# Kernel tuning notes

Hardware: AMD Instinct MI355X
Metric: run time of the kernel (lower is better)

The kernel has to match this reference:

```python
import jax, jax.numpy as jnp
from jax import lax
import numpy as np

B, N, C = 8, 32768, 256          # batch, num votes, seed_feat_dim
P, S = 256, 16                   # num_proposal, nsample
RADIUS = 0.3
NH, NS, NC = 1, 18, 18           # heading bins, size clusters, classes
OUT_DIM = 2 + 3 + NH * 2 + NS * 4 + NC  # 97
BN_EPS = 1e-3                    # keras BatchNormalization default epsilon
BN_SCALE = np.float32(1.0 / np.sqrt(1.0 + BN_EPS))  # moving_mean=0, moving_var=1
MEAN_SIZE = ((np.arange(NS * 3, dtype=np.float32).reshape(NS, 3) % 5.0) + 1.0) * 0.2


def _bn(x, g, b):
    # inference-mode BN with moving_mean=0, moving_var=1
    return g * (x * BN_SCALE) + b


def _fps(xyz, npoint):
    # farthest point sampling -> [B, npoint] int32 indices
    b, n = xyz.shape[0], xyz.shape[1]

    def step(carry, _):
        dist, last = carry                                   # [B,N], [B]
        p = jnp.take_along_axis(xyz, last[:, None, None], axis=1)  # [B,1,3]
        d = jnp.sum((xyz - p) ** 2, axis=-1)                 # [B,N]
        dist = jnp.minimum(dist, d)
        nxt = jnp.argmax(dist, axis=1).astype(jnp.int32)
        return (dist, nxt), last

    init = (jnp.full((b, n), 1e10, xyz.dtype), jnp.zeros((b,), jnp.int32))
    _, inds = lax.scan(step, init, None, length=npoint)
    return jnp.transpose(inds)                               # [B, npoint]


def _ball_query(xyz, new_xyz, radius, nsample):
    # first-nsample neighbors within radius, padded with first hit -> [B,P,S]
    n = xyz.shape[1]
    d2 = (jnp.sum(new_xyz ** 2, -1)[:, :, None]
          + jnp.sum(xyz ** 2, -1)[:, None, :]
          - 2.0 * jnp.einsum('bpd,bnd->bpn', new_xyz, xyz))  # [B,P,N]
    key = jnp.where(d2 < radius * radius, jnp.arange(n, dtype=jnp.int32), n)
    sel = -lax.top_k(-key, nsample)[0]                        # ascending smallest
    first = sel[..., :1]                                      # query point itself is always in-radius
    return jnp.where(sel < n, sel, first)


def _forward(xyz, features, mw0, mb0, mg0, me0, mw1, mb1, mg1, me1,
             mw2, mb2, mg2, me2, hw1, hb1, hg1, he1, hw2, hb2, hg2, he2, hw3, hb3):
    fps_inds = _fps(xyz, P)                                           # [B,P]
    new_xyz = jnp.take_along_axis(xyz, fps_inds[..., None], axis=1)   # [B,P,3]
    idx = _ball_query(xyz, new_xyz, RADIUS, S)                        # [B,P,S]

    g_xyz = jax.vmap(lambda pts, i: pts[i])(xyz, idx)                 # [B,P,S,3]
    g_xyz = (g_xyz - new_xyz[:, :, None, :]) / RADIUS                 # normalize_xyz
    g_feat = jax.vmap(lambda f, i: f[i])(features, idx)               # [B,P,S,C]
    h = jnp.concatenate([g_xyz, g_feat], axis=-1)                     # [B,P,S,C+3]

    # shared MLP (conv2d 1x1 + BN + ReLU) then max-pool over samples
    h = jax.nn.relu(_bn(h @ mw0 + mb0, mg0, me0))
    h = jax.nn.relu(_bn(h @ mw1 + mb1, mg1, me1))
    h = jax.nn.relu(_bn(h @ mw2 + mb2, mg2, me2))
    feats = jnp.max(h, axis=2)                                        # [B,P,128]

    # proposal head: conv1x1 + BN + ReLU x2, then conv1x1
    net = jax.nn.relu(_bn(feats @ hw1 + hb1, hg1, he1))
    net = jax.nn.relu(_bn(net @ hw2 + hb2, hg2, he2))
    net = net @ hw3 + hb3                                             # [B,P,97]

    # decode_scores
    obj = net[:, :, 0:2]
    center = new_xyz + net[:, :, 2:5]
    hs = net[:, :, 5:5 + NH]
    hrn = net[:, :, 5 + NH:5 + 2 * NH]
    hr = hrn * (np.pi / NH)
    ss = net[:, :, 5 + 2 * NH:5 + 2 * NH + NS]
    srn = net[:, :, 5 + 2 * NH + NS:5 + 2 * NH + 4 * NS].reshape(net.shape[0], P, NS, 3)
    sr = srn * jnp.asarray(MEAN_SIZE)[None, None]
    sem = net[:, :, 5 + 2 * NH + 4 * NS:]
    return (obj, center, hs, hrn, hr, ss, srn, sr, sem)


def setup_inputs() -> dict:
    key = jax.random.key(0)
    ks = jax.random.split(key, 16)

    def w(k, shape, scale=0.05):
        return jax.random.normal(k, shape, jnp.float32) * scale

    z, o = jnp.zeros, jnp.ones
    return {
        'xyz': jax.random.normal(ks[0], (B, N, 3), jnp.float32),
        'features': jax.random.normal(ks[1], (B, N, C), jnp.float32),
        'mw0': w(ks[2], (C + 3, 128)), 'mb0': z((128,)), 'mg0': o((128,)), 'me0': z((128,)),
        'mw1': w(ks[3], (128, 128)), 'mb1': z((128,)), 'mg1': o((128,)), 'me1': z((128,)),
        'mw2': w(ks[4], (128, 128)), 'mb2': z((128,)), 'mg2': o((128,)), 'me2': z((128,)),
        'hw1': w(ks[5], (128, 128)), 'hb1': z((128,)), 'hg1': o((128,)), 'he1': z((128,)),
        'hw2': w(ks[6], (128, 128)), 'hb2': z((128,)), 'hg2': o((128,)), 'he2': z((128,)),
        'hw3': w(ks[7], (128, OUT_DIM)), 'hb3': z((OUT_DIM,)),
    }


def reference(xyz, features, mw0, mb0, mg0, me0, mw1, mb1, mg1, me1,
              mw2, mb2, mg2, me2, hw1, hb1, hg1, he1, hw2, hb2, hg2, he2, hw3, hb3):
    return _forward(xyz, features, mw0, mb0, mg0, me0, mw1, mb1, mg1, me1,
                    mw2, mb2, mg2, me2, hw1, hb1, hg1, he1, hw2, hb2, hg2, he2, hw3, hb3)
```

## Files before the change

kernel.cpp:

```cpp
#include <hip/hip_runtime.h>
#include <math.h>

#define NBATCH 8
#define NPOINT 32768
#define NFEAT 256
#define NPROP 256
#define NSAMP 16
#define KIN 259
#define HDIM 128
#define ODIM 97

__device__ __forceinline__ float addrn(float a, float b) {
  float r; asm("v_add_f32 %0, %1, %2" : "=v"(r) : "v"(a), "v"(b)); return r;
}
__device__ __forceinline__ float subrn(float a, float b) {
  float r; asm("v_sub_f32 %0, %1, %2" : "=v"(r) : "v"(a), "v"(b)); return r;
}

__global__ __launch_bounds__(512)
void fps_kernel(const float* __restrict__ xyz, int* __restrict__ fpsi,
                float* __restrict__ cxyz) {
  __shared__ __align__(16) float dist[NPOINT];
  __shared__ float rv[8];
  __shared__ int ri[8];
  __shared__ int bc;
  const int b = blockIdx.x;
  const int t = threadIdx.x;
  const float* __restrict__ Xp = xyz + (size_t)b * NPOINT * 3;
  float px[64], py[64], pz[64];
#pragma unroll
  for (int q = 0; q < 16; ++q) {
#pragma unroll
    for (int u = 0; u < 4; ++u) {
      const int i = q * 2048 + t * 4 + u;
      px[q*4+u] = Xp[3*i+0];
      py[q*4+u] = Xp[3*i+1];
      pz[q*4+u] = Xp[3*i+2];
    }
    *(float4*)&dist[q*2048 + t*4] = make_float4(1e10f, 1e10f, 1e10f, 1e10f);
  }
  __syncthreads();
  int last = 0;
  for (int step = 0; step < NPROP; ++step) {
    const float qx = Xp[3*last+0];
    const float qy = Xp[3*last+1];
    const float qz = Xp[3*last+2];
    if (t == 0) {
      fpsi[b*NPROP + step] = last;
      cxyz[(b*NPROP+step)*3+0] = qx;
      cxyz[(b*NPROP+step)*3+1] = qy;
      cxyz[(b*NPROP+step)*3+2] = qz;
    }
    float bv = -1.0f; int bi = 0;
#pragma unroll
    for (int q = 0; q < 16; ++q) {
      float4 dv = *(float4*)&dist[q*2048 + t*4];
      float* dp = (float*)&dv;
#pragma unroll
      for (int u = 0; u < 4; ++u) {
        const int j = q*4+u;
        const float dx = px[j]-qx, dy = py[j]-qy, dz = pz[j]-qz;
        const float d = addrn(addrn(dx*dx, dy*dy), dz*dz);
        const float nd = fminf(dp[u], d);
        dp[u] = nd;
        if (nd > bv) { bv = nd; bi = q*2048 + t*4 + u; }
      }
      *(float4*)&dist[q*2048 + t*4] = dv;
    }
#pragma unroll
    for (int m = 1; m < 64; m <<= 1) {
      const float ov = __shfl_xor(bv, m);
      const int   oi = __shfl_xor(bi, m);
      if (ov > bv || (ov == bv && oi < bi)) { bv = ov; bi = oi; }
    }
    if ((t & 63) == 0) { rv[t >> 6] = bv; ri[t >> 6] = bi; }
    __syncthreads();
    if (t < 64) {
      float fv = (t < 8) ? rv[t] : -2.0f;
      int   fi = (t < 8) ? ri[t] : 0x7fffffff;
#pragma unroll
      for (int m = 1; m < 8; m <<= 1) {
        const float ov = __shfl_xor(fv, m);
        const int   oi = __shfl_xor(fi, m);
        if (ov > fv || (ov == fv && oi < fi)) { fv = ov; fi = oi; }
      }
      if (t == 0) bc = fi;
    }
    __syncthreads();
    last = bc;
  }
}

__global__ __launch_bounds__(512)
void ballq_kernel(const float* __restrict__ xyz, const float* __restrict__ cxyz,
                  int* __restrict__ idx) {
  const int gw = (blockIdx.x * 512 + threadIdx.x) >> 6;
  const int lane = threadIdx.x & 63;
  const int b = gw >> 8;
  const float* __restrict__ Xp = xyz + (size_t)b * NPOINT * 3;
  const float cx = cxyz[gw*3+0], cy = cxyz[gw*3+1], cz = cxyz[gw*3+2];
  const float a = addrn(addrn(cx*cx, cy*cy), cz*cz);
  const float R2 = (float)(0.3 * 0.3);
  int* __restrict__ out = idx + gw * NSAMP;
  int cnt = 0, first = -1;
  for (int base = 0; base < NPOINT; base += 64) {
    const int i = base + lane;
    const float x = Xp[3*i+0], y = Xp[3*i+1], z = Xp[3*i+2];
    const float bb2 = addrn(addrn(x*x, y*y), z*z);
    const float cc  = addrn(addrn(cx*x, cy*y), cz*z);
    const float d2  = subrn(addrn(a, bb2), 2.0f*cc);
    const bool isin = d2 < R2;
    const unsigned long long m = __ballot(isin);
    if (m) {
      if (first < 0) first = base + (int)__builtin_ctzll(m);
      if (isin) {
        const int pos = cnt + (int)__builtin_popcountll(m & ((1ull << lane) - 1ull));
        if (pos < NSAMP) out[pos] = i;
      }
      cnt += (int)__builtin_popcountll(m);
      if (cnt >= NSAMP) break;
    }
  }
  if (lane < NSAMP && lane >= cnt) out[lane] = first;
}

__global__ __launch_bounds__(256)
void mlp0_kernel(const float* __restrict__ xyz, const float* __restrict__ feat,
                 const float* __restrict__ cxyz, const int* __restrict__ idx,
                 const float* __restrict__ W, const float* __restrict__ bias_,
                 const float* __restrict__ gam_, const float* __restrict__ bet_,
                 float* __restrict__ h0) {
  __shared__ __align__(16) float w[KIN*132];
  __shared__ __align__(16) float xs[16*264];
  __shared__ int ids[16];
  const int t = threadIdx.x;
  for (int i = t; i < KIN*HDIM; i += 256) {
    const int k = i >> 7, c = i & 127;
    w[k*132 + c] = W[i];
  }
  const int r  = t >> 4;
  const int c8 = (t & 15) * 8;
  float bs[8], gm[8], bt[8];
#pragma unroll
  for (int j = 0; j < 8; ++j) { bs[j] = bias_[c8+j]; gm[j] = gam_[c8+j]; bt[j] = bet_[c8+j]; }
  const float bns = (float)(1.0 / sqrt(1.001));
  for (int gi = 0; gi < 8; ++gi) {
    const int g = blockIdx.x * 8 + gi;
    const int b = g >> 8;
    __syncthreads();
    if (t < 16) ids[t] = idx[g*16 + t];
    __syncthreads();
#pragma unroll
    for (int s = 0; s < 16; ++s)
      xs[s*264 + 3 + t] = feat[((size_t)b*NPOINT + ids[s])*NFEAT + t];
    if (t < 48) {
      const int s = t / 3, d = t - 3*(t/3);
      const float v = xyz[((size_t)b*NPOINT + ids[s])*3 + d];
      xs[s*264 + d] = (v - cxyz[g*3 + d]) / 0.3f;
    }
    __syncthreads();
    float acc[8];
#pragma unroll
    for (int j = 0; j < 8; ++j) acc[j] = bs[j];
    for (int k = 0; k < KIN; ++k) {
      const float xv = xs[r*264 + k];
      const float4 wa = *(const float4*)&w[k*132 + c8];
      const float4 wb = *(const float4*)&w[k*132 + c8 + 4];
      acc[0] += xv*wa.x; acc[1] += xv*wa.y; acc[2] += xv*wa.z; acc[3] += xv*wa.w;
      acc[4] += xv*wb.x; acc[5] += xv*wb.y; acc[6] += xv*wb.z; acc[7] += xv*wb.w;
    }
    float ov[8];
#pragma unroll
    for (int j = 0; j < 8; ++j) ov[j] = fmaxf(gm[j]*(acc[j]*bns)+bt[j], 0.0f);
    float* dst = &h0[((size_t)g*16 + r)*HDIM + c8];
    *(float4*)&dst[0] = make_float4(ov[0],ov[1],ov[2],ov[3]);
    *(float4*)&dst[4] = make_float4(ov[4],ov[5],ov[6],ov[7]);
  }
}

__global__ __launch_bounds__(256)
void mlp12_kernel(const float* __restrict__ h0,
                  const float* __restrict__ W1, const float* __restrict__ b1,
                  const float* __restrict__ g1, const float* __restrict__ e1,
                  const float* __restrict__ W2, const float* __restrict__ b2,
                  const float* __restrict__ g2, const float* __restrict__ e2,
                  float* __restrict__ feats) {
  __shared__ __align__(16) float w1[HDIM*132];
  __shared__ __align__(16) float w2[HDIM*132];
  __shared__ __align__(16) float xs[16*132];
  __shared__ __align__(16) float ys[16*132];
  const int t = threadIdx.x;
  for (int i = t; i < HDIM*HDIM; i += 256) {
    const int k = i >> 7, c = i & 127;
    w1[k*132+c] = W1[i];
    w2[k*132+c] = W2[i];
  }
  const int r  = t >> 4;
  const int c8 = (t & 15) * 8;
  float bs1[8], gm1[8], bt1[8], bs2[8], gm2[8], bt2[8];
#pragma unroll
  for (int j = 0; j < 8; ++j) {
    bs1[j]=b1[c8+j]; gm1[j]=g1[c8+j]; bt1[j]=e1[c8+j];
    bs2[j]=b2[c8+j]; gm2[j]=g2[c8+j]; bt2[j]=e2[c8+j];
  }
  const float bns = (float)(1.0 / sqrt(1.001));
  for (int gi = 0; gi < 8; ++gi) {
    const int g = blockIdx.x * 8 + gi;
    __syncthreads();
    for (int i = t; i < 16*HDIM; i += 256) {
      const int s = i >> 7, k = i & 127;
      xs[s*132+k] = h0[((size_t)g*16 + s)*HDIM + k];
    }
    __syncthreads();
    float acc[8];
#pragma unroll
    for (int j = 0; j < 8; ++j) acc[j] = bs1[j];
#pragma unroll 4
    for (int k = 0; k < HDIM; ++k) {
      const float xv = xs[r*132 + k];
      const float4 wa = *(const float4*)&w1[k*132 + c8];
      const float4 wb = *(const float4*)&w1[k*132 + c8 + 4];
      acc[0]+=xv*wa.x; acc[1]+=xv*wa.y; acc[2]+=xv*wa.z; acc[3]+=xv*wa.w;
      acc[4]+=xv*wb.x; acc[5]+=xv*wb.y; acc[6]+=xv*wb.z; acc[7]+=xv*wb.w;
    }
    {
      float ov[8];
#pragma unroll
      for (int j = 0; j < 8; ++j) ov[j] = fmaxf(gm1[j]*(acc[j]*bns)+bt1[j], 0.0f);
      *(float4*)&ys[r*132 + c8]     = make_float4(ov[0],ov[1],ov[2],ov[3]);
      *(float4*)&ys[r*132 + c8 + 4] = make_float4(ov[4],ov[5],ov[6],ov[7]);
    }
    __syncthreads();
#pragma unroll
    for (int j = 0; j < 8; ++j) acc[j] = bs2[j];
#pragma unroll 4
    for (int k = 0; k < HDIM; ++k) {
      const float xv = ys[r*132 + k];
      const float4 wa = *(const float4*)&w2[k*132 + c8];
      const float4 wb = *(const float4*)&w2[k*132 + c8 + 4];
      acc[0]+=xv*wa.x; acc[1]+=xv*wa.y; acc[2]+=xv*wa.z; acc[3]+=xv*wa.w;
      acc[4]+=xv*wb.x; acc[5]+=xv*wb.y; acc[6]+=xv*wb.z; acc[7]+=xv*wb.w;
    }
    {
      float ov[8];
#pragma unroll
      for (int j = 0; j < 8; ++j) ov[j] = fmaxf(gm2[j]*(acc[j]*bns)+bt2[j], 0.0f);
      *(float4*)&xs[r*132 + c8]     = make_float4(ov[0],ov[1],ov[2],ov[3]);
      *(float4*)&xs[r*132 + c8 + 4] = make_float4(ov[4],ov[5],ov[6],ov[7]);
    }
    __syncthreads();
#pragma unroll
    for (int hh = 8; hh >= 1; hh >>= 1) {
      if (r < hh) {
#pragma unroll
        for (int j = 0; j < 8; ++j)
          xs[r*132 + c8 + j] = fmaxf(xs[r*132 + c8 + j], xs[(r+hh)*132 + c8 + j]);
      }
      __syncthreads();
    }
    if (r == 0) {
      *(float4*)&feats[(size_t)g*HDIM + c8]     = *(float4*)&xs[c8];
      *(float4*)&feats[(size_t)g*HDIM + c8 + 4] = *(float4*)&xs[c8+4];
    }
  }
}

__global__ __launch_bounds__(256)
void head_kernel(const float* __restrict__ in_, const float* __restrict__ W,
                 const float* __restrict__ b_, const float* __restrict__ g_,
                 const float* __restrict__ e_, float* __restrict__ out_) {
  __shared__ __align__(16) float w[HDIM*132];
  __shared__ __align__(16) float xs[16*132];
  const int t = threadIdx.x;
  for (int i = t; i < HDIM*HDIM; i += 256) {
    const int k = i >> 7, c = i & 127;
    w[k*132+c] = W[i];
  }
  const int row0 = blockIdx.x * 16;
  for (int i = t; i < 16*HDIM; i += 256) {
    const int s = i >> 7, k = i & 127;
    xs[s*132+k] = in_[((size_t)row0 + s)*HDIM + k];
  }
  const int r  = t >> 4;
  const int c8 = (t & 15) * 8;
  float bs[8], gm[8], bt[8];
#pragma unroll
  for (int j = 0; j < 8; ++j) { bs[j]=b_[c8+j]; gm[j]=g_[c8+j]; bt[j]=e_[c8+j]; }
  const float bns = (float)(1.0 / sqrt(1.001));
  __syncthreads();
  float acc[8];
#pragma unroll
  for (int j = 0; j < 8; ++j) acc[j] = bs[j];
#pragma unroll 4
  for (int k = 0; k < HDIM; ++k) {
    const float xv = xs[r*132 + k];
    const float4 wa = *(const float4*)&w[k*132 + c8];
    const float4 wb = *(const float4*)&w[k*132 + c8 + 4];
    acc[0]+=xv*wa.x; acc[1]+=xv*wa.y; acc[2]+=xv*wa.z; acc[3]+=xv*wa.w;
    acc[4]+=xv*wb.x; acc[5]+=xv*wb.y; acc[6]+=xv*wb.z; acc[7]+=xv*wb.w;
  }
  float ov[8];
#pragma unroll
  for (int j = 0; j < 8; ++j) ov[j] = fmaxf(gm[j]*(acc[j]*bns)+bt[j], 0.0f);
  float* dst = &out_[((size_t)row0 + r)*HDIM + c8];
  *(float4*)&dst[0] = make_float4(ov[0],ov[1],ov[2],ov[3]);
  *(float4*)&dst[4] = make_float4(ov[4],ov[5],ov[6],ov[7]);
}

__global__ __launch_bounds__(128)
void head3_kernel(const float* __restrict__ net2, const float* __restrict__ W3,
                  const float* __restrict__ b3, const float* __restrict__ cxyz,
                  float* __restrict__ out) {
  __shared__ float x[HDIM];
  const int g = blockIdx.x;
  const int t = threadIdx.x;
  x[t] = net2[(size_t)g*HDIM + t];
  __syncthreads();
  if (t >= ODIM) return;
  float acc = b3[t];
#pragma unroll 4
  for (int k = 0; k < HDIM; ++k) acc += x[k] * W3[k*ODIM + t];
  const int OBJ=0, CEN=4096, HSo=10240, HRN=12288, HRo=14336,
            SSo=16384, SRN=53248, SRo=163840, SEM=274432;
  if (t < 2)       out[OBJ + g*2 + t] = acc;
  else if (t < 5)  out[CEN + g*3 + (t-2)] = acc + cxyz[g*3 + (t-2)];
  else if (t == 5) out[HSo + g] = acc;
  else if (t == 6) { out[HRN + g] = acc; out[HRo + g] = acc * (float)M_PI; }
  else if (t < 25) out[SSo + g*18 + (t-7)] = acc;
  else if (t < 79) {
    const int m2 = t - 25;
    out[SRN + g*54 + m2] = acc;
    out[SRo + g*54 + m2] = acc * ((float)(m2 % 5 + 1) * 0.2f);
  }
  else             out[SEM + g*18 + (t-79)] = acc;
}

extern "C" void kernel_launch(void* const* d_in, const int* in_sizes, int n_in,
                              void* d_out, int out_size, void* d_ws, size_t ws_size,
                              hipStream_t stream) {
  (void)in_sizes; (void)n_in; (void)out_size; (void)ws_size;
  const float* xyz  = (const float*)d_in[0];
  const float* feat = (const float*)d_in[1];
  const float* mw0 = (const float*)d_in[2];
  const float* mb0 = (const float*)d_in[3];
  const float* mg0 = (const float*)d_in[4];
  const float* me0 = (const float*)d_in[5];
  const float* mw1 = (const float*)d_in[6];
  const float* mb1 = (const float*)d_in[7];
  const float* mg1 = (const float*)d_in[8];
  const float* me1 = (const float*)d_in[9];
  const float* mw2 = (const float*)d_in[10];
  const float* mb2 = (const float*)d_in[11];
  const float* mg2 = (const float*)d_in[12];
  const float* me2 = (const float*)d_in[13];
  const float* hw1 = (const float*)d_in[14];
  const float* hb1 = (const float*)d_in[15];
  const float* hg1 = (const float*)d_in[16];
  const float* he1 = (const float*)d_in[17];
  const float* hw2 = (const float*)d_in[18];
  const float* hb2 = (const float*)d_in[19];
  const float* hg2 = (const float*)d_in[20];
  const float* he2 = (const float*)d_in[21];
  const float* hw3 = (const float*)d_in[22];
  const float* hb3 = (const float*)d_in[23];
  float* out = (float*)d_out;
  char* ws = (char*)d_ws;
  int*   fpsi = (int*)(ws + 0);
  float* cxyz = (float*)(ws + 8192);
  int*   idx  = (int*)(ws + 32768);
  float* h0   = (float*)(ws + 163840);
  float* fts  = (float*)(ws + 16941056);
  float* net1 = (float*)(ws + 17989632);
  float* net2 = (float*)(ws + 19038208);

  fps_kernel<<<NBATCH, 512, 0, stream>>>(xyz, fpsi, cxyz);
  ballq_kernel<<<256, 512, 0, stream>>>(xyz, cxyz, idx);
  mlp0_kernel<<<256, 256, 0, stream>>>(xyz, feat, cxyz, idx, mw0, mb0, mg0, me0, h0);
  mlp12_kernel<<<256, 256, 0, stream>>>(h0, mw1, mb1, mg1, me1, mw2, mb2, mg2, me2, fts);
  head_kernel<<<128, 256, 0, stream>>>(fts, hw1, hb1, hg1, he1, net1);
  head_kernel<<<128, 256, 0, stream>>>(net1, hw2, hb2, hg2, he2, net2);
  head3_kernel<<<2048, 128, 0, stream>>>(net2, hw3, hb3, cxyz, out);
}
```

Before: 1.284 ms.

## Convert xyz to SoA buffers and widen FPS blocks to 1024 threads

Adds a pre-pass that splits the interleaved xyz array into separate x, y and z arrays in workspace. FPS and ball query then read them with coalesced, vectorized float4 loads and single-element lookups instead of strided loads. FPS now uses 1024 threads per batch, so each thread holds 32 points instead of 64 and the cross-wave reduction covers 16 waves. The cost is an extra kernel launch plus the SoA write and read traffic. The SoA buffers alias the h0 region, which is written only later by mlp0, and the unused fps index output is dropped.

```diff
diff --git a/kernel.cpp b/kernel.cpp
--- a/kernel.cpp
+++ b/kernel.cpp
@@ -17,44 +17,55 @@
   float r; asm("v_sub_f32 %0, %1, %2" : "=v"(r) : "v"(a), "v"(b)); return r;
 }
 
-__global__ __launch_bounds__(512)
-void fps_kernel(const float* __restrict__ xyz, int* __restrict__ fpsi,
-                float* __restrict__ cxyz) {
+__global__ __launch_bounds__(256)
+void soa_kernel(const float* __restrict__ xyz, float* __restrict__ xs,
+                float* __restrict__ ys, float* __restrict__ zs) {
+  const int i = blockIdx.x * 256 + threadIdx.x;
+  xs[i] = xyz[3*i+0];
+  ys[i] = xyz[3*i+1];
+  zs[i] = xyz[3*i+2];
+}
+
+__global__ __launch_bounds__(1024, 4)
+void fps_kernel(const float* __restrict__ xs_, const float* __restrict__ ys_,
+                const float* __restrict__ zs_, float* __restrict__ cxyz) {
   __shared__ __align__(16) float dist[NPOINT];
-  __shared__ float rv[8];
-  __shared__ int ri[8];
+  __shared__ float rv[16];
+  __shared__ int ri[16];
   __shared__ int bc;
   const int b = blockIdx.x;
   const int t = threadIdx.x;
-  const float* __restrict__ Xp = xyz + (size_t)b * NPOINT * 3;
-  float px[64], py[64], pz[64];
-#pragma unroll
-  for (int q = 0; q < 16; ++q) {
-#pragma unroll
-    for (int u = 0; u < 4; ++u) {
-      const int i = q * 2048 + t * 4 + u;
-      px[q*4+u] = Xp[3*i+0];
-      py[q*4+u] = Xp[3*i+1];
-      pz[q*4+u] = Xp[3*i+2];
-    }
-    *(float4*)&dist[q*2048 + t*4] = make_float4(1e10f, 1e10f, 1e10f, 1e10f);
+  const float* __restrict__ X = xs_ + (size_t)b * NPOINT;
+  const float* __restrict__ Y = ys_ + (size_t)b * NPOINT;
+  const float* __restrict__ Z = zs_ + (size_t)b * NPOINT;
+  float px[32], py[32], pz[32];
+#pragma unroll
+  for (int q = 0; q < 8; ++q) {
+    const int o = q * 4096 + t * 4;
+    const float4 vx = *(const float4*)&X[o];
+    const float4 vy = *(const float4*)&Y[o];
+    const float4 vz = *(const float4*)&Z[o];
+    px[q*4+0]=vx.x; px[q*4+1]=vx.y; px[q*4+2]=vx.z; px[q*4+3]=vx.w;
+    py[q*4+0]=vy.x; py[q*4+1]=vy.y; py[q*4+2]=vy.z; py[q*4+3]=vy.w;
+    pz[q*4+0]=vz.x; pz[q*4+1]=vz.y; pz[q*4+2]=vz.z; pz[q*4+3]=vz.w;
+    *(float4*)&dist[o] = make_float4(1e10f, 1e10f, 1e10f, 1e10f);
   }
   __syncthreads();
   int last = 0;
   for (int step = 0; step < NPROP; ++step) {
-    const float qx = Xp[3*last+0];
-    const float qy = Xp[3*last+1];
-    const float qz = Xp[3*last+2];
+    const float qx = X[last];
+    const float qy = Y[last];
+    const float qz = Z[last];
     if (t == 0) {
-      fpsi[b*NPROP + step] = last;
       cxyz[(b*NPROP+step)*3+0] = qx;
       cxyz[(b*NPROP+step)*3+1] = qy;
       cxyz[(b*NPROP+step)*3+2] = qz;
     }
     float bv = -1.0f; int bi = 0;
 #pragma unroll
-    for (int q = 0; q < 16; ++q) {
-      float4 dv = *(float4*)&dist[q*2048 + t*4];
+    for (int q = 0; q < 8; ++q) {
+      const int o = q * 4096 + t * 4;
+      float4 dv = *(float4*)&dist[o];
       float* dp = (float*)&dv;
 #pragma unroll
       for (int u = 0; u < 4; ++u) {
@@ -63,9 +74,9 @@
         const float d = addrn(addrn(dx*dx, dy*dy), dz*dz);
         const float nd = fminf(dp[u], d);
         dp[u] = nd;
-        if (nd > bv) { bv = nd; bi = q*2048 + t*4 + u; }
+        if (nd > bv) { bv = nd; bi = o + u; }
       }
-      *(float4*)&dist[q*2048 + t*4] = dv;
+      *(float4*)&dist[o] = dv;
     }
 #pragma unroll
     for (int m = 1; m < 64; m <<= 1) {
@@ -76,10 +87,10 @@
     if ((t & 63) == 0) { rv[t >> 6] = bv; ri[t >> 6] = bi; }
     __syncthreads();
     if (t < 64) {
-      float fv = (t < 8) ? rv[t] : -2.0f;
-      int   fi = (t < 8) ? ri[t] : 0x7fffffff;
-#pragma unroll
-      for (int m = 1; m < 8; m <<= 1) {
+      float fv = (t < 16) ? rv[t] : -2.0f;
+      int   fi = (t < 16) ? ri[t] : 0x7fffffff;
+#pragma unroll
+      for (int m = 1; m < 16; m <<= 1) {
         const float ov = __shfl_xor(fv, m);
         const int   oi = __shfl_xor(fi, m);
         if (ov > fv || (ov == fv && oi < fi)) { fv = ov; fi = oi; }
@@ -92,12 +103,15 @@
 }
 
 __global__ __launch_bounds__(512)
-void ballq_kernel(const float* __restrict__ xyz, const float* __restrict__ cxyz,
+void ballq_kernel(const float* __restrict__ xs_, const float* __restrict__ ys_,
+                  const float* __restrict__ zs_, const float* __restrict__ cxyz,
                   int* __restrict__ idx) {
   const int gw = (blockIdx.x * 512 + threadIdx.x) >> 6;
   const int lane = threadIdx.x & 63;
   const int b = gw >> 8;
-  const float* __restrict__ Xp = xyz + (size_t)b * NPOINT * 3;
+  const float* __restrict__ X = xs_ + (size_t)b * NPOINT;
+  const float* __restrict__ Y = ys_ + (size_t)b * NPOINT;
+  const float* __restrict__ Z = zs_ + (size_t)b * NPOINT;
   const float cx = cxyz[gw*3+0], cy = cxyz[gw*3+1], cz = cxyz[gw*3+2];
   const float a = addrn(addrn(cx*cx, cy*cy), cz*cz);
   const float R2 = (float)(0.3 * 0.3);
@@ -105,7 +119,7 @@
   int cnt = 0, first = -1;
   for (int base = 0; base < NPOINT; base += 64) {
     const int i = base + lane;
-    const float x = Xp[3*i+0], y = Xp[3*i+1], z = Xp[3*i+2];
+    const float x = X[i], y = Y[i], z = Z[i];
     const float bb2 = addrn(addrn(x*x, y*y), z*z);
     const float cc  = addrn(addrn(cx*x, cy*y), cz*z);
     const float d2  = subrn(addrn(a, bb2), 2.0f*cc);
@@ -365,16 +379,19 @@
   const float* hb3 = (const float*)d_in[23];
   float* out = (float*)d_out;
   char* ws = (char*)d_ws;
-  int*   fpsi = (int*)(ws + 0);
   float* cxyz = (float*)(ws + 8192);
   int*   idx  = (int*)(ws + 32768);
   float* h0   = (float*)(ws + 163840);
+  float* xs   = (float*)(ws + 163840);
+  float* ys   = (float*)(ws + 163840 + 1048576);
+  float* zs   = (float*)(ws + 163840 + 2097152);
   float* fts  = (float*)(ws + 16941056);
   float* net1 = (float*)(ws + 17989632);
   float* net2 = (float*)(ws + 19038208);
 
-  fps_kernel<<<NBATCH, 512, 0, stream>>>(xyz, fpsi, cxyz);
-  ballq_kernel<<<256, 512, 0, stream>>>(xyz, cxyz, idx);
+  soa_kernel<<<1024, 256, 0, stream>>>(xyz, xs, ys, zs);
+  fps_kernel<<<NBATCH, 1024, 0, stream>>>(xs, ys, zs, cxyz);
+  ballq_kernel<<<256, 512, 0, stream>>>(xs, ys, zs, cxyz, idx);
   mlp0_kernel<<<256, 256, 0, stream>>>(xyz, feat, cxyz, idx, mw0, mb0, mg0, me0, h0);
   mlp12_kernel<<<256, 256, 0, stream>>>(h0, mw1, mb1, mg1, me1, mw2, mb2, mg2, me2, fts);
   head_kernel<<<128, 256, 0, stream>>>(fts, hw1, hb1, hg1, he1, net1);
```

Measured after the change: 1.309 ms. About the same (+1.9%).
